# Kernel tuning notes

Measured on AMD Instinct MI355X. Metric: run time of the kernel, lower is better.

## Reference

```python
import jax, jax.numpy as jnp
import numpy as np

D_MODEL = 2048
N_HEADS = 16
HEAD_DIM = D_MODEL // N_HEADS
SEGMENT_SIZE = 512
DILATION = 2
BATCH = 2
SEQ_LEN = 8192


def setup_inputs() -> dict:
    key = jax.random.key(0)
    k1, k2, k3 = jax.random.split(key, 3)
    x = jax.random.normal(k1, (BATCH, SEQ_LEN, D_MODEL), dtype=jnp.float32)
    Wqkv = jax.random.normal(k2, (3 * D_MODEL, D_MODEL), dtype=jnp.float32) * 0.02
    b_qkv = jnp.zeros((3 * D_MODEL,), dtype=jnp.float32)
    Wout = jax.random.normal(k3, (D_MODEL, D_MODEL), dtype=jnp.float32) * 0.02
    b_out = jnp.zeros((D_MODEL,), dtype=jnp.float32)
    return {"x": x, "Wqkv": Wqkv, "b_qkv": b_qkv, "Wout": Wout, "b_out": b_out}


def reference(x, Wqkv, b_qkv, Wout, b_out):
    B, S, D = x.shape
    H, hd = N_HEADS, HEAD_DIM
    # dilated segment gather: [B, n_seg, seg, D] strided by dilation -> [B, n_seg, L, D]
    xs = x.reshape(B, -1, SEGMENT_SIZE, D)[:, :, ::DILATION, :]
    N, L = xs.shape[1], xs.shape[2]
    # fused qkv projection (FlashMHA.Wqkv)
    qkv = jnp.einsum('bnld,ed->bnle', xs, Wqkv) + b_qkv  # [B,N,L,3D]
    q, k, v = jnp.split(qkv, 3, axis=-1)
    q = q.reshape(B, N, L, H, hd)
    k = k.reshape(B, N, L, H, hd)
    v = v.reshape(B, N, L, H, hd)
    scale = 1.0 / jnp.sqrt(jnp.asarray(hd, dtype=x.dtype))
    # per-segment attention over the dilated tokens
    scores = jnp.einsum('bnqhd,bnkhd->bnhqk', q, k) * scale  # [B,N,H,L,L]
    attn = jax.nn.softmax(scores, axis=-1)
    out = jnp.einsum('bnhqk,bnkhd->bnqhd', attn, v).reshape(B, N, L, D)
    # output projection (FlashMHA.out_proj)
    out = jnp.einsum('bnld,ed->bnle', out, Wout) + b_out
    # merge segments back: [B, N*L, D]
    return out.reshape(B, -1, D)
```

## Files before the change

### kernel.cpp

```cpp
#include <hip/hip_runtime.h>
#include <hip/hip_bf16.h>
#include <stdint.h>

#define DEVI __device__ __forceinline__

typedef __attribute__((ext_vector_type(8))) short bf16x8;
typedef __attribute__((ext_vector_type(4))) float f32x4;


DEVI unsigned short f2bf(float f) {
  unsigned int u = __float_as_uint(f);
  return (unsigned short)((u + 0x7fffu + ((u >> 16) & 1u)) >> 16);
}

DEVI void load_lds16(const void* g, void* l) {
  __builtin_amdgcn_global_load_lds(
      (const __attribute__((address_space(1))) unsigned int*)g,
      (__attribute__((address_space(3))) unsigned int*)l, 16, 0, 0);
}

DEVI bf16x8 ld8(const unsigned short* p) {
  return *reinterpret_cast<const bf16x8*>(p);
}

__global__ void k_prep(const float* __restrict__ x, unsigned short* __restrict__ xs,
                       const float* __restrict__ Wqkv, unsigned short* __restrict__ wq,
                       const float* __restrict__ Wout, unsigned short* __restrict__ wo) {
  const int bid = blockIdx.x;
  const float* src;
  unsigned short* dst;
  long i;
  if (bid < 16384) {
    int ii = bid * 256 + threadIdx.x;
    int r = ii >> 9;
    int c = (ii & 511) << 2;
    int b = r >> 12;
    int rem = r & 4095;
    int seg = rem >> 8;
    int lcl = rem & 255;
    long src_row = (long)b * 8192 + seg * 512 + lcl * 2;
    const float4 v = *reinterpret_cast<const float4*>(x + src_row * 2048 + c);
    uint2 o;
    o.x = f2bf(v.x) | ((unsigned)f2bf(v.y) << 16);
    o.y = f2bf(v.z) | ((unsigned)f2bf(v.w) << 16);
    *reinterpret_cast<uint2*>(xs + (long)r * 2048 + c) = o;
    return;
  } else if (bid < 28672) {
    i = (long)(bid - 16384) * 256 + threadIdx.x;
    src = Wqkv; dst = wq;
  } else {
    i = (long)(bid - 28672) * 256 + threadIdx.x;
    src = Wout; dst = wo;
  }
  const float4 v = *reinterpret_cast<const float4*>(src + i * 4);
  uint2 o;
  o.x = f2bf(v.x) | ((unsigned)f2bf(v.y) << 16);
  o.y = f2bf(v.z) | ((unsigned)f2bf(v.w) << 16);
  *reinterpret_cast<uint2*>(dst + i * 4) = o;
}


DEVI long stage_off(int s, int K) {
  int prow = s >> 3;
  int cs8 = s & 7;
  int c8 = cs8 ^ (prow & 7);
  int r = prow * 2 + (c8 >> 2);
  int k0 = (c8 & 3) << 3;
  return (long)r * K + k0;
}

#define FRAG_A(dst, mm)                                                      \
  { int r_ = wm * 128 + (mm) * 16 + lr;                                      \
    int p_ = r_ >> 1;                                                        \
    int cs_ = (((r_ & 1) << 2) | lq) ^ (p_ & 7);                             \
    dst = ld8(Ab_ + p_ * 64 + cs_ * 8); }
#define FRAG_B(dst, nn)                                                      \
  { int r_ = wn * 64 + (nn) * 16 + lr;                                       \
    int p_ = r_ >> 1;                                                        \
    int cs_ = (((r_ & 1) << 2) | lq) ^ (p_ & 7);                             \
    dst = ld8(Bb_ + p_ * 64 + cs_ * 8); }

#define STAGE_J(j)                                                           \
    load_lds16(pA0 + (j) * 32, (char*)smem + (((j) + 3) & 3) * 32768 + w * 1024);          \
    load_lds16(pA1 + (j) * 32, (char*)smem + (((j) + 3) & 3) * 32768 + 8192 + w * 1024);   \
    load_lds16(pB0 + (j) * 32, (char*)smem + (((j) + 3) & 3) * 32768 + 16384 + w * 1024);  \
    load_lds16(pB1 + (j) * 32, (char*)smem + (((j) + 3) & 3) * 32768 + 24576 + w * 1024);

#define HALF_J(j, DOSTAGE, VMLIT)                                            \
  {                                                                          \
    const unsigned short* Ab_ = smem + ((j) & 3) * 16384;                    \
    const unsigned short* Bb_ = Ab_ + 8192;                                  \
    if (DOSTAGE) { STAGE_J(j) }                                              \
    bf16x8 bfr[4], afr[8];                                                   \
    FRAG_B(bfr[0], 0) FRAG_B(bfr[1], 1) FRAG_B(bfr[2], 2) FRAG_B(bfr[3], 3)  \
    FRAG_A(afr[0], 0) FRAG_A(afr[1], 1) FRAG_A(afr[2], 2) FRAG_A(afr[3], 3)  \
    FRAG_A(afr[4], 4) FRAG_A(afr[5], 5) FRAG_A(afr[6], 6) FRAG_A(afr[7], 7)  \
    _Pragma("unroll")                                                        \
    for (int m_ = 0; m_ < 8; ++m_)                                           \
      _Pragma("unroll")                                                      \
      for (int n_ = 0; n_ < 4; ++n_)                                         \
        acc[m_][n_] = __builtin_amdgcn_mfma_f32_16x16x32_bf16(               \
            afr[m_], bfr[n_], acc[m_][n_], 0, 0, 0);                         \
    asm volatile("s_waitcnt vmcnt(" VMLIT ")" ::: "memory");                 \
    __builtin_amdgcn_s_barrier();                                            \
    asm volatile("" ::: "memory");                                           \
  }

template <bool BF16_OUT>
__global__ __launch_bounds__(512, 1)
void k_gemm(const unsigned short* __restrict__ A, const unsigned short* __restrict__ B,
            const float* __restrict__ bias, void* __restrict__ Cv, int N,
            int CHY, int CHX) {
  constexpr int K = 2048;
  __shared__ unsigned short smem[65536];
  const int nbx = N >> 8;
  const int xcd = blockIdx.x & 7;
  const int local = blockIdx.x >> 3;
  const int nchx = nbx / CHX;
  const int by = (xcd / nchx) * CHY + local / CHX;
  const int bx = (xcd % nchx) * CHX + local % CHX;
  const int t = threadIdx.x, w = t >> 6, l = t & 63;
  const int lr = l & 15, lq = l >> 4;
  const int wm = w >> 2, wn = w & 3;
  const unsigned short* Agb = A + (long)by * 256 * K;
  const unsigned short* Bgb = B + (long)bx * 256 * K;
  f32x4 acc[8][4] = {};

  const unsigned short* pA0 = Agb + stage_off(t, K);
  const unsigned short* pA1 = Agb + stage_off(512 + t, K);
  const unsigned short* pB0 = Bgb + stage_off(t, K);
  const unsigned short* pB1 = Bgb + stage_off(512 + t, K);

  load_lds16(pA0, (char*)smem + w * 1024);
  load_lds16(pA1, (char*)smem + 8192 + w * 1024);
  load_lds16(pB0, (char*)smem + 16384 + w * 1024);
  load_lds16(pB1, (char*)smem + 24576 + w * 1024);
  load_lds16(pA0 + 32, (char*)smem + 32768 + w * 1024);
  load_lds16(pA1 + 32, (char*)smem + 32768 + 8192 + w * 1024);
  load_lds16(pB0 + 32, (char*)smem + 32768 + 16384 + w * 1024);
  load_lds16(pB1 + 32, (char*)smem + 32768 + 24576 + w * 1024);
  load_lds16(pA0 + 64, (char*)smem + 65536 + w * 1024);
  load_lds16(pA1 + 64, (char*)smem + 65536 + 8192 + w * 1024);
  load_lds16(pB0 + 64, (char*)smem + 65536 + 16384 + w * 1024);
  load_lds16(pB1 + 64, (char*)smem + 65536 + 24576 + w * 1024);
  pA0 += 96; pA1 += 96; pB0 += 96; pB1 += 96;
  asm volatile("s_waitcnt vmcnt(8)" ::: "memory");
  __builtin_amdgcn_s_barrier();
  asm volatile("" ::: "memory");

  for (int hg = 0; hg < 15; ++hg) {
    HALF_J(0, true, "8") HALF_J(1, true, "8")
    HALF_J(2, true, "8") HALF_J(3, true, "8")
    pA0 += 128; pA1 += 128; pB0 += 128; pB1 += 128;
  }
  HALF_J(0, true, "8")
  HALF_J(1, false, "4")
  HALF_J(2, false, "0")
  HALF_J(3, false, "0")

  const long crow0 = (long)by * 256 + wm * 128;
  const int ccol0 = bx * 256 + wn * 64;
  float bv[4];
#pragma unroll
  for (int n = 0; n < 4; ++n) bv[n] = bias[ccol0 + n * 16 + lr];
  const int lrr = l >> 2;
  if (BF16_OUT) {
    unsigned short* Lw = smem + w * 1216;
    const int lcb = (l & 3) * 8;
#pragma unroll
    for (int m = 0; m < 8; ++m) {
#pragma unroll
      for (int n = 0; n < 4; ++n)
#pragma unroll
        for (int r = 0; r < 4; ++r)
          Lw[(lq * 4 + r) * 76 + n * 16 + lr] = f2bf(acc[m][n][r] + bv[n]);
      asm volatile("s_waitcnt lgkmcnt(0)" ::: "memory");
#pragma unroll
      for (int rd = 0; rd < 2; ++rd) {
        bf16x8 v = ld8(Lw + lrr * 76 + lcb + rd * 32);
        *reinterpret_cast<bf16x8*>((unsigned short*)Cv +
            (crow0 + m * 16 + lrr) * N + ccol0 + lcb + rd * 32) = v;
      }
    }
  } else {
    float* Lf = (float*)smem + w * 1216;
    const int lcf = (l & 3) * 4;
#pragma unroll
    for (int m = 0; m < 8; ++m) {
#pragma unroll
      for (int n = 0; n < 4; ++n)
#pragma unroll
        for (int r = 0; r < 4; ++r)
          Lf[(lq * 4 + r) * 76 + n * 16 + lr] = acc[m][n][r] + bv[n];
      asm volatile("s_waitcnt lgkmcnt(0)" ::: "memory");
#pragma unroll
      for (int rd = 0; rd < 4; ++rd) {
        float4 v = *reinterpret_cast<const float4*>(Lf + lrr * 76 + lcf + rd * 16);
        *reinterpret_cast<float4*>((float*)Cv +
            (crow0 + m * 16 + lrr) * N + ccol0 + lcf + rd * 16) = v;
      }
    }
  }
}

__global__ __launch_bounds__(512)
void k_attn(const unsigned short* __restrict__ qkv, unsigned short* __restrict__ aout) {
  __shared__ unsigned short smem[65536];
  unsigned short* Kl = smem;
  unsigned short* Vt = smem + 32768;
  const int p = blockIdx.x;
  const int h = p & 15;
  const long rb = (long)(p >> 4) * 256;
  const int t = threadIdx.x, w = t >> 6, l = t & 63;
  const int lr = l & 15, lq = l >> 4;

  const unsigned short* kb = qkv + rb * 6144 + 2048 + h * 128;
#pragma unroll
  for (int i = 0; i < 8; ++i) {
    int s = i * 512 + t;
    int row = s >> 4;
    int ch = (s & 15) ^ (row & 7);
    load_lds16(kb + (long)row * 6144 + ch * 8, (char*)Kl + i * 8192 + w * 1024);
  }
  const unsigned short* vb = qkv + rb * 6144 + 4096 + h * 128;
#pragma unroll
  for (int j0 = 0; j0 < 8; ++j0) {
    int k = j0 * 32 + (t >> 4);
    int d0 = (t & 15) * 8;
    bf16x8 v = ld8(vb + (long)k * 6144 + d0);
#pragma unroll
    for (int j = 0; j < 8; ++j) {
      int d = d0 + j;
      int ch = (k >> 3) ^ ((d ^ (d >> 3)) & 7);
      Vt[d * 256 + ch * 8 + (k & 7)] = (unsigned short)(short)v[j];
    }
  }
  const unsigned short* qb = qkv + (rb + w * 32) * 6144 + h * 128;
  bf16x8 qa[2][4];
#pragma unroll
  for (int m = 0; m < 2; ++m)
#pragma unroll
    for (int kt = 0; kt < 4; ++kt)
      qa[m][kt] = ld8(qb + (long)(m * 16 + lr) * 6144 + kt * 32 + lq * 8);

  __syncthreads();

  f32x4 sacc[2][16] = {};
#pragma unroll
  for (int n = 0; n < 16; ++n) {
    int row = n * 16 + lr;
#pragma unroll
    for (int kt = 0; kt < 4; ++kt) {
      int ch = (kt * 4 + lq) ^ (row & 7);
      bf16x8 kf = ld8(Kl + row * 128 + ch * 8);
      sacc[0][n] = __builtin_amdgcn_mfma_f32_16x16x32_bf16(qa[0][kt], kf, sacc[0][n], 0, 0, 0);
      sacc[1][n] = __builtin_amdgcn_mfma_f32_16x16x32_bf16(qa[1][kt], kf, sacc[1][n], 0, 0, 0);
    }
  }
  const float scale = 0.08838834764831845f;
  float mx[2][4], sm[2][4];
#pragma unroll
  for (int m = 0; m < 2; ++m)
#pragma unroll
    for (int r = 0; r < 4; ++r) {
      float v = sacc[m][0][r];
#pragma unroll
      for (int n = 1; n < 16; ++n) v = fmaxf(v, sacc[m][n][r]);
      mx[m][r] = v;
      sm[m][r] = 0.f;
    }
#pragma unroll
  for (int mk = 1; mk < 16; mk <<= 1)
#pragma unroll
    for (int m = 0; m < 2; ++m)
#pragma unroll
      for (int r = 0; r < 4; ++r)
        mx[m][r] = fmaxf(mx[m][r], __shfl_xor(mx[m][r], mk));
#pragma unroll
  for (int m = 0; m < 2; ++m)
#pragma unroll
    for (int n = 0; n < 16; ++n)
#pragma unroll
      for (int r = 0; r < 4; ++r) {
        float e = __expf((sacc[m][n][r] - mx[m][r]) * scale);
        sacc[m][n][r] = e;
        sm[m][r] += e;
      }
#pragma unroll
  for (int mk = 1; mk < 16; mk <<= 1)
#pragma unroll
    for (int m = 0; m < 2; ++m)
#pragma unroll
      for (int r = 0; r < 4; ++r)
        sm[m][r] += __shfl_xor(sm[m][r], mk);
  float ri[2][4];
#pragma unroll
  for (int m = 0; m < 2; ++m)
#pragma unroll
    for (int r = 0; r < 4; ++r) ri[m][r] = 1.0f / sm[m][r];

  unsigned int pb[2][16][2];
#pragma unroll
  for (int m = 0; m < 2; ++m)
#pragma unroll
    for (int n = 0; n < 16; ++n) {
      pb[m][n][0] = f2bf(sacc[m][n][0] * ri[m][0]) | ((unsigned)f2bf(sacc[m][n][1] * ri[m][1]) << 16);
      pb[m][n][1] = f2bf(sacc[m][n][2] * ri[m][2]) | ((unsigned)f2bf(sacc[m][n][3] * ri[m][3]) << 16);
    }

  __syncthreads();
  unsigned short* Pl = Kl + w * 4096;
  f32x4 oacc[2][8] = {};
#pragma unroll
  for (int half = 0; half < 2; ++half) {
#pragma unroll
    for (int m = 0; m < 2; ++m)
#pragma unroll
      for (int n = 0; n < 8; ++n) {
        int col = n * 16 + lr;
        int row0 = m * 16 + lq * 4;
#pragma unroll
        for (int pr = 0; pr < 2; ++pr) {
          unsigned int u = pb[m][half * 8 + n][pr];
          int ra = row0 + pr * 2, rbw = ra + 1;
          int ca = (col >> 3) ^ (ra & 7);
          int cb = (col >> 3) ^ (rbw & 7);
          Pl[ra * 128 + ca * 8 + (col & 7)] = (unsigned short)(u & 0xffffu);
          Pl[rbw * 128 + cb * 8 + (col & 7)] = (unsigned short)(u >> 16);
        }
      }
#pragma unroll
    for (int kt = 0; kt < 4; ++kt) {
      bf16x8 pa[2];
#pragma unroll
      for (int m = 0; m < 2; ++m) {
        int row = m * 16 + lr;
        int ch = (kt * 4 + lq) ^ (row & 7);
        pa[m] = ld8(Pl + row * 128 + ch * 8);
      }
#pragma unroll
      for (int dt = 0; dt < 8; ++dt) {
        int d = dt * 16 + lr;
        int kg = half * 128 + kt * 32 + lq * 8;
        int ch = (kg >> 3) ^ ((d ^ (d >> 3)) & 7);
        bf16x8 vf = ld8(Vt + d * 256 + ch * 8);
        oacc[0][dt] = __builtin_amdgcn_mfma_f32_16x16x32_bf16(pa[0], vf, oacc[0][dt], 0, 0, 0);
        oacc[1][dt] = __builtin_amdgcn_mfma_f32_16x16x32_bf16(pa[1], vf, oacc[1][dt], 0, 0, 0);
      }
    }
  }
  unsigned short* ob = aout + (rb + w * 32) * 2048 + h * 128;
#pragma unroll
  for (int m = 0; m < 2; ++m)
#pragma unroll
    for (int dt = 0; dt < 8; ++dt)
#pragma unroll
      for (int r = 0; r < 4; ++r)
        ob[(long)(m * 16 + lq * 4 + r) * 2048 + dt * 16 + lr] = f2bf(oacc[m][dt][r]);
}

extern "C" void kernel_launch(void* const* d_in, const int* in_sizes, int n_in,
                              void* d_out, int out_size, void* d_ws, size_t ws_size,
                              hipStream_t stream) {
  const float* x     = (const float*)d_in[0];
  const float* Wqkv  = (const float*)d_in[1];
  const float* b_qkv = (const float*)d_in[2];
  const float* Wout  = (const float*)d_in[3];
  const float* b_out = (const float*)d_in[4];
  float* out = (float*)d_out;

  char* ws = (char*)d_ws;
  unsigned short* xs   = (unsigned short*)(ws);
  unsigned short* aout = xs;
  unsigned short* wq   = (unsigned short*)(ws + 33554432);
  unsigned short* wo   = (unsigned short*)(ws + 58720256);
  unsigned short* qkv  = (unsigned short*)(ws + 67108864);

  k_prep<<<32768, 256, 0, stream>>>(x, xs, Wqkv, wq, Wout, wo);
  k_gemm<true><<<768, 512, 0, stream>>>(xs, wq, b_qkv, (void*)qkv, 6144, 16, 6);
  k_attn<<<512, 512, 0, stream>>>(qkv, aout);
  k_gemm<false><<<256, 512, 0, stream>>>(aout, wo, b_out, (void*)out, 2048, 8, 4);
}
```

Measured before the change: 323.6 us.

## Shrink GEMM tile to 256x128 with three-stage LDS pipeline

```diff
diff --git a/kernel.cpp b/kernel.cpp
--- a/kernel.cpp
+++ b/kernel.cpp
@@ -75,32 +75,41 @@
     int cs_ = (((r_ & 1) << 2) | lq) ^ (p_ & 7);                             \
     dst = ld8(Ab_ + p_ * 64 + cs_ * 8); }
 #define FRAG_B(dst, nn)                                                      \
-  { int r_ = wn * 64 + (nn) * 16 + lr;                                       \
+  { int r_ = wn * 32 + (nn) * 16 + lr;                                       \
     int p_ = r_ >> 1;                                                        \
     int cs_ = (((r_ & 1) << 2) | lq) ^ (p_ & 7);                             \
     dst = ld8(Bb_ + p_ * 64 + cs_ * 8); }
 
-#define STAGE_J(j)                                                           \
-    load_lds16(pA0 + (j) * 32, (char*)smem + (((j) + 3) & 3) * 32768 + w * 1024);          \
-    load_lds16(pA1 + (j) * 32, (char*)smem + (((j) + 3) & 3) * 32768 + 8192 + w * 1024);   \
-    load_lds16(pB0 + (j) * 32, (char*)smem + (((j) + 3) & 3) * 32768 + 16384 + w * 1024);  \
-    load_lds16(pB1 + (j) * 32, (char*)smem + (((j) + 3) & 3) * 32768 + 24576 + w * 1024);
-
-#define HALF_J(j, DOSTAGE, VMLIT)                                            \
+#define HALF3(j, DOSTAGE, VMLIT)                                             \
   {                                                                          \
-    const unsigned short* Ab_ = smem + ((j) & 3) * 16384;                    \
+    const unsigned short* Ab_ = smem + (j) * 12288;                          \
     const unsigned short* Bb_ = Ab_ + 8192;                                  \
-    if (DOSTAGE) { STAGE_J(j) }                                              \
-    bf16x8 bfr[4], afr[8];                                                   \
-    FRAG_B(bfr[0], 0) FRAG_B(bfr[1], 1) FRAG_B(bfr[2], 2) FRAG_B(bfr[3], 3)  \
-    FRAG_A(afr[0], 0) FRAG_A(afr[1], 1) FRAG_A(afr[2], 2) FRAG_A(afr[3], 3)  \
-    FRAG_A(afr[4], 4) FRAG_A(afr[5], 5) FRAG_A(afr[6], 6) FRAG_A(afr[7], 7)  \
-    _Pragma("unroll")                                                        \
-    for (int m_ = 0; m_ < 8; ++m_)                                           \
-      _Pragma("unroll")                                                      \
-      for (int n_ = 0; n_ < 4; ++n_)                                         \
-        acc[m_][n_] = __builtin_amdgcn_mfma_f32_16x16x32_bf16(               \
-            afr[m_], bfr[n_], acc[m_][n_], 0, 0, 0);                         \
+    if (DOSTAGE) {                                                           \
+      char* tgt = (char*)smem + (((j) + 2) % 3) * 24576;                     \
+      load_lds16(pA0 + (j) * 32, tgt + w * 1024);                            \
+      load_lds16(pA1 + (j) * 32, tgt + 8192 + w * 1024);                     \
+      load_lds16(pB0 + (j) * 32, tgt + 16384 + w * 1024);                    \
+    }                                                                        \
+    bf16x8 bfr0, bfr1, af0, af1, af2, af3;                                   \
+    FRAG_B(bfr0, 0) FRAG_B(bfr1, 1)                                          \
+    FRAG_A(af0, 0) FRAG_A(af1, 1) FRAG_A(af2, 2) FRAG_A(af3, 3)              \
+    acc[0][0] = __builtin_amdgcn_mfma_f32_16x16x32_bf16(af0, bfr0, acc[0][0], 0, 0, 0); \
+    acc[0][1] = __builtin_amdgcn_mfma_f32_16x16x32_bf16(af0, bfr1, acc[0][1], 0, 0, 0); \
+    acc[1][0] = __builtin_amdgcn_mfma_f32_16x16x32_bf16(af1, bfr0, acc[1][0], 0, 0, 0); \
+    acc[1][1] = __builtin_amdgcn_mfma_f32_16x16x32_bf16(af1, bfr1, acc[1][1], 0, 0, 0); \
+    acc[2][0] = __builtin_amdgcn_mfma_f32_16x16x32_bf16(af2, bfr0, acc[2][0], 0, 0, 0); \
+    acc[2][1] = __builtin_amdgcn_mfma_f32_16x16x32_bf16(af2, bfr1, acc[2][1], 0, 0, 0); \
+    acc[3][0] = __builtin_amdgcn_mfma_f32_16x16x32_bf16(af3, bfr0, acc[3][0], 0, 0, 0); \
+    acc[3][1] = __builtin_amdgcn_mfma_f32_16x16x32_bf16(af3, bfr1, acc[3][1], 0, 0, 0); \
+    FRAG_A(af0, 4) FRAG_A(af1, 5) FRAG_A(af2, 6) FRAG_A(af3, 7)              \
+    acc[4][0] = __builtin_amdgcn_mfma_f32_16x16x32_bf16(af0, bfr0, acc[4][0], 0, 0, 0); \
+    acc[4][1] = __builtin_amdgcn_mfma_f32_16x16x32_bf16(af0, bfr1, acc[4][1], 0, 0, 0); \
+    acc[5][0] = __builtin_amdgcn_mfma_f32_16x16x32_bf16(af1, bfr0, acc[5][0], 0, 0, 0); \
+    acc[5][1] = __builtin_amdgcn_mfma_f32_16x16x32_bf16(af1, bfr1, acc[5][1], 0, 0, 0); \
+    acc[6][0] = __builtin_amdgcn_mfma_f32_16x16x32_bf16(af2, bfr0, acc[6][0], 0, 0, 0); \
+    acc[6][1] = __builtin_amdgcn_mfma_f32_16x16x32_bf16(af2, bfr1, acc[6][1], 0, 0, 0); \
+    acc[7][0] = __builtin_amdgcn_mfma_f32_16x16x32_bf16(af3, bfr0, acc[7][0], 0, 0, 0); \
+    acc[7][1] = __builtin_amdgcn_mfma_f32_16x16x32_bf16(af3, bfr1, acc[7][1], 0, 0, 0); \
     asm volatile("s_waitcnt vmcnt(" VMLIT ")" ::: "memory");                 \
     __builtin_amdgcn_s_barrier();                                            \
     asm volatile("" ::: "memory");                                           \
@@ -112,8 +121,8 @@
             const float* __restrict__ bias, void* __restrict__ Cv, int N,
             int CHY, int CHX) {
   constexpr int K = 2048;
-  __shared__ unsigned short smem[65536];
-  const int nbx = N >> 8;
+  __shared__ unsigned short smem[36864];
+  const int nbx = N >> 7;
   const int xcd = blockIdx.x & 7;
   const int local = blockIdx.x >> 3;
   const int nchx = nbx / CHX;
@@ -123,79 +132,68 @@
   const int lr = l & 15, lq = l >> 4;
   const int wm = w >> 2, wn = w & 3;
   const unsigned short* Agb = A + (long)by * 256 * K;
-  const unsigned short* Bgb = B + (long)bx * 256 * K;
-  f32x4 acc[8][4] = {};
+  const unsigned short* Bgb = B + (long)bx * 128 * K;
+  f32x4 acc[8][2] = {};
 
   const unsigned short* pA0 = Agb + stage_off(t, K);
   const unsigned short* pA1 = Agb + stage_off(512 + t, K);
   const unsigned short* pB0 = Bgb + stage_off(t, K);
-  const unsigned short* pB1 = Bgb + stage_off(512 + t, K);
 
   load_lds16(pA0, (char*)smem + w * 1024);
   load_lds16(pA1, (char*)smem + 8192 + w * 1024);
   load_lds16(pB0, (char*)smem + 16384 + w * 1024);
-  load_lds16(pB1, (char*)smem + 24576 + w * 1024);
-  load_lds16(pA0 + 32, (char*)smem + 32768 + w * 1024);
-  load_lds16(pA1 + 32, (char*)smem + 32768 + 8192 + w * 1024);
-  load_lds16(pB0 + 32, (char*)smem + 32768 + 16384 + w * 1024);
-  load_lds16(pB1 + 32, (char*)smem + 32768 + 24576 + w * 1024);
-  load_lds16(pA0 + 64, (char*)smem + 65536 + w * 1024);
-  load_lds16(pA1 + 64, (char*)smem + 65536 + 8192 + w * 1024);
-  load_lds16(pB0 + 64, (char*)smem + 65536 + 16384 + w * 1024);
-  load_lds16(pB1 + 64, (char*)smem + 65536 + 24576 + w * 1024);
-  pA0 += 96; pA1 += 96; pB0 += 96; pB1 += 96;
-  asm volatile("s_waitcnt vmcnt(8)" ::: "memory");
+  load_lds16(pA0 + 32, (char*)smem + 24576 + w * 1024);
+  load_lds16(pA1 + 32, (char*)smem + 24576 + 8192 + w * 1024);
+  load_lds16(pB0 + 32, (char*)smem + 24576 + 16384 + w * 1024);
+  pA0 += 64; pA1 += 64; pB0 += 64;
+  asm volatile("s_waitcnt vmcnt(3)" ::: "memory");
   __builtin_amdgcn_s_barrier();
   asm volatile("" ::: "memory");
 
-  for (int hg = 0; hg < 15; ++hg) {
-    HALF_J(0, true, "8") HALF_J(1, true, "8")
-    HALF_J(2, true, "8") HALF_J(3, true, "8")
-    pA0 += 128; pA1 += 128; pB0 += 128; pB1 += 128;
-  }
-  HALF_J(0, true, "8")
-  HALF_J(1, false, "4")
-  HALF_J(2, false, "0")
-  HALF_J(3, false, "0")
+  for (int hg = 0; hg < 20; ++hg) {
+    HALF3(0, true, "3") HALF3(1, true, "3") HALF3(2, true, "3")
+    pA0 += 96; pA1 += 96; pB0 += 96;
+  }
+  HALF3(0, true, "3")
+  HALF3(1, true, "3")
+  HALF3(2, false, "0")
+  HALF3(0, false, "0")
 
   const long crow0 = (long)by * 256 + wm * 128;
-  const int ccol0 = bx * 256 + wn * 64;
-  float bv[4];
-#pragma unroll
-  for (int n = 0; n < 4; ++n) bv[n] = bias[ccol0 + n * 16 + lr];
+  const int ccol0 = bx * 128 + wn * 32;
+  float bv[2];
+#pragma unroll
+  for (int n = 0; n < 2; ++n) bv[n] = bias[ccol0 + n * 16 + lr];
   const int lrr = l >> 2;
   if (BF16_OUT) {
-    unsigned short* Lw = smem + w * 1216;
+    unsigned short* Lw = smem + w * 640;
     const int lcb = (l & 3) * 8;
 #pragma unroll
     for (int m = 0; m < 8; ++m) {
 #pragma unroll
-      for (int n = 0; n < 4; ++n)
+      for (int n = 0; n < 2; ++n)
 #pragma unroll
         for (int r = 0; r < 4; ++r)
-          Lw[(lq * 4 + r) * 76 + n * 16 + lr] = f2bf(acc[m][n][r] + bv[n]);
+          Lw[(lq * 4 + r) * 40 + n * 16 + lr] = f2bf(acc[m][n][r] + bv[n]);
       asm volatile("s_waitcnt lgkmcnt(0)" ::: "memory");
+      bf16x8 v = ld8(Lw + lrr * 40 + lcb);
+      *reinterpret_cast<bf16x8*>((unsigned short*)Cv +
+          (crow0 + m * 16 + lrr) * N + ccol0 + lcb) = v;
+    }
+  } else {
+    float* Lf = (float*)smem + w * 576;
+    const int lcf = (l & 3) * 4;
+#pragma unroll
+    for (int m = 0; m < 8; ++m) {
+#pragma unroll
+      for (int n = 0; n < 2; ++n)
+#pragma unroll
+        for (int r = 0; r < 4; ++r)
+          Lf[(lq * 4 + r) * 36 + n * 16 + lr] = acc[m][n][r] + bv[n];
+      asm volatile("s_waitcnt lgkmcnt(0)" ::: "memory");
 #pragma unroll
       for (int rd = 0; rd < 2; ++rd) {
-        bf16x8 v = ld8(Lw + lrr * 76 + lcb + rd * 32);
-        *reinterpret_cast<bf16x8*>((unsigned short*)Cv +
-            (crow0 + m * 16 + lrr) * N + ccol0 + lcb + rd * 32) = v;
-      }
-    }
-  } else {
-    float* Lf = (float*)smem + w * 1216;
-    const int lcf = (l & 3) * 4;
-#pragma unroll
-    for (int m = 0; m < 8; ++m) {
-#pragma unroll
-      for (int n = 0; n < 4; ++n)
-#pragma unroll
-        for (int r = 0; r < 4; ++r)
-          Lf[(lq * 4 + r) * 76 + n * 16 + lr] = acc[m][n][r] + bv[n];
-      asm volatile("s_waitcnt lgkmcnt(0)" ::: "memory");
-#pragma unroll
-      for (int rd = 0; rd < 4; ++rd) {
-        float4 v = *reinterpret_cast<const float4*>(Lf + lrr * 76 + lcf + rd * 16);
+        float4 v = *reinterpret_cast<const float4*>(Lf + lrr * 36 + lcf + rd * 16);
         *reinterpret_cast<float4*>((float*)Cv +
             (crow0 + m * 16 + lrr) * N + ccol0 + lcf + rd * 16) = v;
       }
@@ -377,7 +375,7 @@
   unsigned short* qkv  = (unsigned short*)(ws + 67108864);
 
   k_prep<<<32768, 256, 0, stream>>>(x, xs, Wqkv, wq, Wout, wo);
-  k_gemm<true><<<768, 512, 0, stream>>>(xs, wq, b_qkv, (void*)qkv, 6144, 16, 6);
+  k_gemm<true><<<1536, 512, 0, stream>>>(xs, wq, b_qkv, (void*)qkv, 6144, 16, 12);
   k_attn<<<512, 512, 0, stream>>>(qkv, aout);
-  k_gemm<false><<<256, 512, 0, stream>>>(aout, wo, b_out, (void*)out, 2048, 8, 4);
-}
+  k_gemm<false><<<512, 512, 0, stream>>>(aout, wo, b_out, (void*)out, 2048, 8, 8);
+}
```

After: 365.6 us. 13.0% more time.

## Pair K-steps per barrier in GEMM pipeline and raise priority around attention MFMAs

Applied to the files above, without the earlier changes.

```diff
diff --git a/kernel.cpp b/kernel.cpp
--- a/kernel.cpp
+++ b/kernel.cpp
@@ -80,17 +80,17 @@
     int cs_ = (((r_ & 1) << 2) | lq) ^ (p_ & 7);                             \
     dst = ld8(Bb_ + p_ * 64 + cs_ * 8); }
 
-#define STAGE_J(j)                                                           \
-    load_lds16(pA0 + (j) * 32, (char*)smem + (((j) + 3) & 3) * 32768 + w * 1024);          \
-    load_lds16(pA1 + (j) * 32, (char*)smem + (((j) + 3) & 3) * 32768 + 8192 + w * 1024);   \
-    load_lds16(pB0 + (j) * 32, (char*)smem + (((j) + 3) & 3) * 32768 + 16384 + w * 1024);  \
-    load_lds16(pB1 + (j) * 32, (char*)smem + (((j) + 3) & 3) * 32768 + 24576 + w * 1024);
-
-#define HALF_J(j, DOSTAGE, VMLIT)                                            \
+#define HALF_BODY(SLOT, STG, POFF)                                           \
   {                                                                          \
-    const unsigned short* Ab_ = smem + ((j) & 3) * 16384;                    \
+    const unsigned short* Ab_ = smem + (SLOT) * 16384;                       \
     const unsigned short* Bb_ = Ab_ + 8192;                                  \
-    if (DOSTAGE) { STAGE_J(j) }                                              \
+    if (STG) {                                                               \
+      char* tgt_ = (char*)smem + (((SLOT) + 2) & 3) * 32768;                 \
+      load_lds16(pA0 + (POFF), tgt_ + w * 1024);                             \
+      load_lds16(pA1 + (POFF), tgt_ + 8192 + w * 1024);                      \
+      load_lds16(pB0 + (POFF), tgt_ + 16384 + w * 1024);                     \
+      load_lds16(pB1 + (POFF), tgt_ + 24576 + w * 1024);                     \
+    }                                                                        \
     bf16x8 bfr[4], afr[8];                                                   \
     FRAG_B(bfr[0], 0) FRAG_B(bfr[1], 1) FRAG_B(bfr[2], 2) FRAG_B(bfr[3], 3)  \
     FRAG_A(afr[0], 0) FRAG_A(afr[1], 1) FRAG_A(afr[2], 2) FRAG_A(afr[3], 3)  \
@@ -101,10 +101,14 @@
       for (int n_ = 0; n_ < 4; ++n_)                                         \
         acc[m_][n_] = __builtin_amdgcn_mfma_f32_16x16x32_bf16(               \
             afr[m_], bfr[n_], acc[m_][n_], 0, 0, 0);                         \
-    asm volatile("s_waitcnt vmcnt(" VMLIT ")" ::: "memory");                 \
-    __builtin_amdgcn_s_barrier();                                            \
-    asm volatile("" ::: "memory");                                           \
-  }
+  }
+
+#define PAIRM(SA, SB, STG, OFFA, OFFB)                                       \
+  HALF_BODY(SA, STG, OFFA)                                                   \
+  HALF_BODY(SB, STG, OFFB)                                                   \
+  asm volatile("s_waitcnt vmcnt(0)" ::: "memory");                           \
+  __builtin_amdgcn_s_barrier();                                              \
+  asm volatile("" ::: "memory");
 
 template <bool BF16_OUT>
 __global__ __launch_bounds__(512, 1)
@@ -139,24 +143,19 @@
   load_lds16(pA1 + 32, (char*)smem + 32768 + 8192 + w * 1024);
   load_lds16(pB0 + 32, (char*)smem + 32768 + 16384 + w * 1024);
   load_lds16(pB1 + 32, (char*)smem + 32768 + 24576 + w * 1024);
-  load_lds16(pA0 + 64, (char*)smem + 65536 + w * 1024);
-  load_lds16(pA1 + 64, (char*)smem + 65536 + 8192 + w * 1024);
-  load_lds16(pB0 + 64, (char*)smem + 65536 + 16384 + w * 1024);
-  load_lds16(pB1 + 64, (char*)smem + 65536 + 24576 + w * 1024);
-  pA0 += 96; pA1 += 96; pB0 += 96; pB1 += 96;
-  asm volatile("s_waitcnt vmcnt(8)" ::: "memory");
+  pA0 += 64; pA1 += 64; pB0 += 64;
+  pB1 += 64;
+  asm volatile("s_waitcnt vmcnt(0)" ::: "memory");
   __builtin_amdgcn_s_barrier();
   asm volatile("" ::: "memory");
 
   for (int hg = 0; hg < 15; ++hg) {
-    HALF_J(0, true, "8") HALF_J(1, true, "8")
-    HALF_J(2, true, "8") HALF_J(3, true, "8")
+    PAIRM(0, 1, true, 0, 32)
+    PAIRM(2, 3, true, 64, 96)
     pA0 += 128; pA1 += 128; pB0 += 128; pB1 += 128;
   }
-  HALF_J(0, true, "8")
-  HALF_J(1, false, "4")
-  HALF_J(2, false, "0")
-  HALF_J(3, false, "0")
+  PAIRM(0, 1, true, 0, 32)
+  PAIRM(2, 3, false, 0, 0)
 
   const long crow0 = (long)by * 256 + wm * 128;
   const int ccol0 = bx * 256 + wn * 64;
@@ -246,6 +245,7 @@
   __syncthreads();
 
   f32x4 sacc[2][16] = {};
+  __builtin_amdgcn_s_setprio(1);
 #pragma unroll
   for (int n = 0; n < 16; ++n) {
     int row = n * 16 + lr;
@@ -257,6 +257,7 @@
       sacc[1][n] = __builtin_amdgcn_mfma_f32_16x16x32_bf16(qa[1][kt], kf, sacc[1][n], 0, 0, 0);
     }
   }
+  __builtin_amdgcn_s_setprio(0);
   const float scale = 0.08838834764831845f;
   float mx[2][4], sm[2][4];
 #pragma unroll
@@ -329,6 +330,7 @@
           Pl[rbw * 128 + cb * 8 + (col & 7)] = (unsigned short)(u >> 16);
         }
       }
+    __builtin_amdgcn_s_setprio(1);
 #pragma unroll
     for (int kt = 0; kt < 4; ++kt) {
       bf16x8 pa[2];
@@ -348,6 +350,7 @@
         oacc[1][dt] = __builtin_amdgcn_mfma_f32_16x16x32_bf16(pa[1], vf, oacc[1][dt], 0, 0, 0);
       }
     }
+    __builtin_amdgcn_s_setprio(0);
   }
   unsigned short* ob = aout + (rb + w * 32) * 2048 + h * 128;
 #pragma unroll
```

Result: slower. 338.8 us (+4.7%).
